# Kernel tuning notes

Measured on AMD Instinct MI355X. Metric: run time of the kernel, lower is better.

The kernel has to match this reference:

```python
import jax, jax.numpy as jnp
import numpy as np

SEQ, D_IN, D_OUT = 8192, 1024, 1024


def setup_inputs() -> dict:
    key = jax.random.key(0)
    kx, kq, kk, kv = jax.random.split(key, 4)
    # torch nn.Linear weights have shape (out_features, in_features)
    s = 1.0 / np.sqrt(D_IN)
    return {
        "x": jax.random.normal(kx, (SEQ, D_IN), dtype=jnp.float32),
        "Wq": jax.random.uniform(kq, (D_OUT, D_IN), dtype=jnp.float32, minval=-s, maxval=s),
        "Wk": jax.random.uniform(kk, (D_OUT, D_IN), dtype=jnp.float32, minval=-s, maxval=s),
        "Wv": jax.random.uniform(kv, (D_OUT, D_IN), dtype=jnp.float32, minval=-s, maxval=s),
    }


def reference(x, Wq, Wk, Wv):
    # Linear (no bias): y = x @ W.T
    q = x @ Wq.T          # [S, D_OUT]
    k = x @ Wk.T          # [S, D_OUT]
    v = x @ Wv.T          # [S, D_OUT]
    scale = 1.0 / jnp.sqrt(jnp.asarray(k.shape[-1], dtype=x.dtype))
    scores = (q @ k.T) * scale            # [S, S]
    weights = jax.nn.softmax(scores, axis=-1)
    return weights @ v                    # [S, D_OUT]
```

## Files before the change

### kernel.cpp

```cpp
#include <hip/hip_runtime.h>
#include <hip/hip_bf16.h>
#include <stdint.h>


#define SEQ 8192
#define DMODEL 1024
#define LOG2E 1.44269504088896340736f
#define GROUP_M 8

typedef __bf16 bf16_t;
typedef __bf16 bf16x8 __attribute__((ext_vector_type(8)));
typedef float f32x4 __attribute__((ext_vector_type(4)));

__global__ __launch_bounds__(256)
void convert_f32_bf16(const float* __restrict__ in, bf16_t* __restrict__ out, long n) {
    long i = ((long)blockIdx.x * 256 + threadIdx.x) * 4;
    if (i + 3 < n) {
        const float4 v = *(const float4*)(in + i);
        union { ushort4 u; bf16_t b[4]; } p;
        p.b[0] = (bf16_t)v.x; p.b[1] = (bf16_t)v.y;
        p.b[2] = (bf16_t)v.z; p.b[3] = (bf16_t)v.w;
        *(ushort4*)(out + i) = p.u;
    }
}

__global__ __launch_bounds__(256)
void add_f32(float* __restrict__ out, const float* __restrict__ part, long n) {
    long i = ((long)blockIdx.x * 256 + threadIdx.x) * 4;
    if (i + 3 < n) {
        float4 a = *(const float4*)(out + i);
        const float4 b = *(const float4*)(part + i);
        a.x += b.x; a.y += b.y; a.z += b.z; a.w += b.w;
        *(float4*)(out + i) = a;
    }
}

template <typename OutT>
__global__ __launch_bounds__(256, 3)
void gemm_nt(const bf16_t* __restrict__ A, const bf16_t* __restrict__ B,
             OutT* __restrict__ C0, OutT* __restrict__ C1,
             int M, int N, int Kps, int lda, int ldb, int ldc, float alpha)
{
    __shared__ bf16_t As[128 * 32];
    __shared__ bf16_t Bs[128 * 32];

    const int tid  = threadIdx.x;
    const int wave = tid >> 6;
    const int lane = tid & 63;

    const int nbm = M >> 7, nbn = N >> 7;
    const int tiles = nbm * nbn;
    int bid = blockIdx.x;
    const int sid = bid / tiles;
    bid -= sid * tiles;
    const long kbase = (long)sid * Kps;
    OutT* __restrict__ C = sid ? C1 : C0;

    const int per_group = GROUP_M * nbn;
    const int gid   = bid / per_group;
    const int rem   = bid - gid * per_group;
    const int first = gid * GROUP_M;
    const int gsz   = min(nbm - first, GROUP_M);
    const int bm    = first + rem % gsz;
    const int bn    = rem / gsz;
    const long row0 = (long)bm * 128;
    const long col0 = (long)bn * 128;

    const int wm = (wave >> 1) * 64;
    const int wn = (wave & 1) * 64;
    const int lr = lane & 15;
    const int lq = lane >> 4;

    f32x4 acc[4][4] = {};

    for (int k0 = 0; k0 < Kps; k0 += 32) {
        #pragma unroll
        for (int i = 0; i < 2; ++i) {
            const int cbase = i * 256 + wave * 64;
            const int c = cbase + lane;
            const int r = c >> 2, cc = c & 3;
            const bf16_t* ga = A + (row0 + r) * (long)lda + kbase + k0 + cc * 8;
            const bf16_t* gb = B + (col0 + r) * (long)ldb + kbase + k0 + cc * 8;
            __builtin_amdgcn_global_load_lds(
                (const __attribute__((address_space(1))) uint32_t*)ga,
                (__attribute__((address_space(3))) uint32_t*)(As + (long)cbase * 8),
                16, 0, 0);
            __builtin_amdgcn_global_load_lds(
                (const __attribute__((address_space(1))) uint32_t*)gb,
                (__attribute__((address_space(3))) uint32_t*)(Bs + (long)cbase * 8),
                16, 0, 0);
        }
        __syncthreads();

        bf16x8 af[4], bfr[4];
        #pragma unroll
        for (int mi = 0; mi < 4; ++mi)
            af[mi] = *(const bf16x8*)(As + (wm + mi * 16 + lr) * 32 + lq * 8);
        #pragma unroll
        for (int ni = 0; ni < 4; ++ni)
            bfr[ni] = *(const bf16x8*)(Bs + (wn + ni * 16 + lr) * 32 + lq * 8);

        #pragma unroll
        for (int mi = 0; mi < 4; ++mi)
            #pragma unroll
            for (int ni = 0; ni < 4; ++ni)
                acc[mi][ni] = __builtin_amdgcn_mfma_f32_16x16x32_bf16(
                    af[mi], bfr[ni], acc[mi][ni], 0, 0, 0);
        __syncthreads();
    }

    #pragma unroll
    for (int mi = 0; mi < 4; ++mi)
        #pragma unroll
        for (int ni = 0; ni < 4; ++ni)
            #pragma unroll
            for (int rg = 0; rg < 4; ++rg) {
                const long r = row0 + wm + mi * 16 + lq * 4 + rg;
                const long c = col0 + wn + ni * 16 + lr;
                C[r * (long)ldc + c] = (OutT)(alpha * acc[mi][ni][rg]);
            }
}

__global__ __launch_bounds__(256)
void transpose_bf16(const bf16_t* __restrict__ in, bf16_t* __restrict__ out,
                    int R, int ldin, int ldout)
{
    __shared__ bf16_t tile[32][33];
    const int tx = threadIdx.x & 31;
    const int ty = threadIdx.x >> 5;
    const int c0 = blockIdx.x * 32;
    const int r0 = blockIdx.y * 32;
    #pragma unroll
    for (int j = 0; j < 32; j += 8)
        tile[ty + j][tx] = in[(long)(r0 + ty + j) * ldin + c0 + tx];
    __syncthreads();
    #pragma unroll
    for (int j = 0; j < 32; j += 8)
        out[(long)(c0 + ty + j) * ldout + r0 + tx] = tile[tx][ty + j];
}

__global__ __launch_bounds__(256)
void softmax_rows(bf16_t* __restrict__ S, int n)
{
    const long row = blockIdx.x;
    bf16_t* p = S + row * (long)n;
    const int tid = threadIdx.x;
    const int wave = tid >> 6, lane = tid & 63;
    __shared__ float red[4];

    float v[32];
    #pragma unroll
    for (int j = 0; j < 4; ++j) {
        bf16x8 x = *(const bf16x8*)(p + ((long)(j * 256 + tid)) * 8);
        #pragma unroll
        for (int e = 0; e < 8; ++e) v[j * 8 + e] = (float)x[e];
    }
    float m = -3.4e38f;
    #pragma unroll
    for (int i = 0; i < 32; ++i) m = fmaxf(m, v[i]);
    #pragma unroll
    for (int off = 32; off > 0; off >>= 1) m = fmaxf(m, __shfl_xor(m, off));
    if (lane == 0) red[wave] = m;
    __syncthreads();
    m = fmaxf(fmaxf(red[0], red[1]), fmaxf(red[2], red[3]));
    __syncthreads();

    float s = 0.f;
    #pragma unroll
    for (int i = 0; i < 32; ++i) { v[i] = exp2f((v[i] - m) * LOG2E); s += v[i]; }
    #pragma unroll
    for (int off = 32; off > 0; off >>= 1) s += __shfl_xor(s, off);
    if (lane == 0) red[wave] = s;
    __syncthreads();
    s = red[0] + red[1] + red[2] + red[3];
    const float inv = 1.f / s;

    #pragma unroll
    for (int j = 0; j < 4; ++j) {
        bf16x8 x;
        #pragma unroll
        for (int e = 0; e < 8; ++e) x[e] = (bf16_t)(v[j * 8 + e] * inv);
        *(bf16x8*)(p + ((long)(j * 256 + tid)) * 8) = x;
    }
}

extern "C" void kernel_launch(void* const* d_in, const int* in_sizes, int n_in,
                              void* d_out, int out_size, void* d_ws, size_t ws_size,
                              hipStream_t stream)
{
    const float* x  = (const float*)d_in[0];
    const float* Wq = (const float*)d_in[1];
    const float* Wk = (const float*)d_in[2];
    const float* Wv = (const float*)d_in[3];
    float* out = (float*)d_out;

    char* ws = (char*)d_ws;
    const long XN = (long)SEQ * DMODEL;
    const long WN = (long)DMODEL * DMODEL;
    const long SN = (long)SEQ * SEQ;

    bf16_t* xb   = (bf16_t*)ws;
    bf16_t* wcat = (bf16_t*)(ws + XN * 2);
    bf16_t* qkv  = (bf16_t*)(ws + XN * 2 + WN * 6);
    bf16_t* Sb   = (bf16_t*)(ws + XN * 2 + WN * 6 + XN * 6);
    float*  pvp  = (float*)(ws + XN * 2 + WN * 6 + XN * 6 + SN * 2);
    bf16_t* vtb  = xb;

    const size_t need_split = (size_t)(XN * 2 + WN * 6 + XN * 6 + SN * 2) + XN * 4;
    const bool use_split = ws_size >= need_split;

    convert_f32_bf16<<<(int)(XN / 4 / 256), 256, 0, stream>>>(x,  xb, XN);
    convert_f32_bf16<<<(int)(WN / 4 / 256), 256, 0, stream>>>(Wq, wcat,          WN);
    convert_f32_bf16<<<(int)(WN / 4 / 256), 256, 0, stream>>>(Wk, wcat + WN,     WN);
    convert_f32_bf16<<<(int)(WN / 4 / 256), 256, 0, stream>>>(Wv, wcat + 2 * WN, WN);

    dim3 blk(256);
    gemm_nt<bf16_t><<<(SEQ / 128) * (3 * DMODEL / 128), blk, 0, stream>>>(
        xb, wcat, qkv, qkv, SEQ, 3 * DMODEL, DMODEL,
        DMODEL, DMODEL, 3 * DMODEL, 1.0f);

    bf16_t* qb = qkv;
    bf16_t* kb = qkv + DMODEL;
    bf16_t* vb = qkv + 2 * DMODEL;

    transpose_bf16<<<dim3(DMODEL / 32, SEQ / 32), blk, 0, stream>>>(
        vb, vtb, SEQ, 3 * DMODEL, SEQ);

    gemm_nt<bf16_t><<<(SEQ / 128) * (SEQ / 128), blk, 0, stream>>>(
        qb, kb, Sb, Sb, SEQ, SEQ, DMODEL,
        3 * DMODEL, 3 * DMODEL, SEQ, 0.03125f);

    softmax_rows<<<SEQ, blk, 0, stream>>>(Sb, SEQ);

    if (use_split) {
        gemm_nt<float><<<2 * (SEQ / 128) * (DMODEL / 128), blk, 0, stream>>>(
            Sb, vtb, out, pvp, SEQ, DMODEL, SEQ / 2,
            SEQ, SEQ, DMODEL, 1.0f);
        add_f32<<<(int)(XN / 4 / 256), 256, 0, stream>>>(out, pvp, XN);
    } else {
        gemm_nt<float><<<(SEQ / 128) * (DMODEL / 128), blk, 0, stream>>>(
            Sb, vtb, out, out, SEQ, DMODEL, SEQ,
            SEQ, SEQ, DMODEL, 1.0f);
    }
}
```

Baseline: 564.6 us.

## Compute QK^T scores with FP8 MFMA using e4m3 Q/K from fused QKV epilogue

The QKV projection kernel now writes Q and K as FP8 e4m3 and V as bf16 into separate planes. A new FP8 GEMM then computes the 8192x8192 score matrix using the fp8 16x16x32 MFMA with 64-wide K tiles. The aim is to double the math throughput and halve the operand bandwidth of the largest GEMM. In exchange, FP8 precision for Q and K reduces score accuracy, and there is no per-tensor scaling.

```diff
diff --git a/kernel.cpp b/kernel.cpp
--- a/kernel.cpp
+++ b/kernel.cpp
@@ -11,6 +11,11 @@
 typedef __bf16 bf16_t;
 typedef __bf16 bf16x8 __attribute__((ext_vector_type(8)));
 typedef float f32x4 __attribute__((ext_vector_type(4)));
+
+__device__ __forceinline__ uint8_t f32_to_e4m3(float v) {
+    int p = __builtin_amdgcn_cvt_pk_fp8_f32(v, 0.0f, 0, false);
+    return (uint8_t)(p & 0xff);
+}
 
 __global__ __launch_bounds__(256)
 void convert_f32_bf16(const float* __restrict__ in, bf16_t* __restrict__ out, long n) {
@@ -35,6 +40,172 @@
     }
 }
 
+__global__ __launch_bounds__(256, 3)
+void gemm_qkv(const bf16_t* __restrict__ A, const bf16_t* __restrict__ B,
+              uint8_t* __restrict__ qf8, uint8_t* __restrict__ kf8,
+              bf16_t* __restrict__ vb)
+{
+    __shared__ bf16_t As[128 * 32];
+    __shared__ bf16_t Bs[128 * 32];
+
+    const int tid  = threadIdx.x;
+    const int wave = tid >> 6;
+    const int lane = tid & 63;
+
+    const int nbm = SEQ >> 7, nbn = (3 * DMODEL) >> 7;
+    const int per_group = GROUP_M * nbn;
+    const int gid   = blockIdx.x / per_group;
+    const int rem   = blockIdx.x - gid * per_group;
+    const int first = gid * GROUP_M;
+    const int gsz   = min(nbm - first, GROUP_M);
+    const int bm    = first + rem % gsz;
+    const int bn    = rem / gsz;
+    const long row0 = (long)bm * 128;
+    const long col0 = (long)bn * 128;
+
+    const int wm = (wave >> 1) * 64;
+    const int wn = (wave & 1) * 64;
+    const int lr = lane & 15;
+    const int lq = lane >> 4;
+
+    f32x4 acc[4][4] = {};
+
+    for (int k0 = 0; k0 < DMODEL; k0 += 32) {
+        #pragma unroll
+        for (int i = 0; i < 2; ++i) {
+            const int cbase = i * 256 + wave * 64;
+            const int c = cbase + lane;
+            const int r = c >> 2, cc = c & 3;
+            const bf16_t* ga = A + (row0 + r) * (long)DMODEL + k0 + cc * 8;
+            const bf16_t* gb = B + (col0 + r) * (long)DMODEL + k0 + cc * 8;
+            __builtin_amdgcn_global_load_lds(
+                (const __attribute__((address_space(1))) uint32_t*)ga,
+                (__attribute__((address_space(3))) uint32_t*)(As + (long)cbase * 8),
+                16, 0, 0);
+            __builtin_amdgcn_global_load_lds(
+                (const __attribute__((address_space(1))) uint32_t*)gb,
+                (__attribute__((address_space(3))) uint32_t*)(Bs + (long)cbase * 8),
+                16, 0, 0);
+        }
+        __syncthreads();
+
+        bf16x8 af[4], bfr[4];
+        #pragma unroll
+        for (int mi = 0; mi < 4; ++mi)
+            af[mi] = *(const bf16x8*)(As + (wm + mi * 16 + lr) * 32 + lq * 8);
+        #pragma unroll
+        for (int ni = 0; ni < 4; ++ni)
+            bfr[ni] = *(const bf16x8*)(Bs + (wn + ni * 16 + lr) * 32 + lq * 8);
+
+        #pragma unroll
+        for (int mi = 0; mi < 4; ++mi)
+            #pragma unroll
+            for (int ni = 0; ni < 4; ++ni)
+                acc[mi][ni] = __builtin_amdgcn_mfma_f32_16x16x32_bf16(
+                    af[mi], bfr[ni], acc[mi][ni], 0, 0, 0);
+        __syncthreads();
+    }
+
+    const int plane = (int)(col0 >> 10);
+    const int cb    = (int)(col0 & 1023);
+    #pragma unroll
+    for (int mi = 0; mi < 4; ++mi)
+        #pragma unroll
+        for (int ni = 0; ni < 4; ++ni)
+            #pragma unroll
+            for (int rg = 0; rg < 4; ++rg) {
+                const long r = row0 + wm + mi * 16 + lq * 4 + rg;
+                const int  c = cb + wn + ni * 16 + lr;
+                const float val = acc[mi][ni][rg];
+                if (plane == 2)
+                    vb[r * (long)DMODEL + c] = (bf16_t)val;
+                else if (plane == 1)
+                    kf8[r * (long)DMODEL + c] = f32_to_e4m3(val);
+                else
+                    qf8[r * (long)DMODEL + c] = f32_to_e4m3(val);
+            }
+}
+
+__global__ __launch_bounds__(256, 3)
+void gemm_s_fp8(const uint8_t* __restrict__ A, const uint8_t* __restrict__ B,
+                bf16_t* __restrict__ C, float alpha)
+{
+    __shared__ uint8_t As[128 * 64];
+    __shared__ uint8_t Bs[128 * 64];
+
+    const int tid  = threadIdx.x;
+    const int wave = tid >> 6;
+    const int lane = tid & 63;
+
+    const int nbm = SEQ >> 7, nbn = SEQ >> 7;
+    const int per_group = GROUP_M * nbn;
+    const int gid   = blockIdx.x / per_group;
+    const int rem   = blockIdx.x - gid * per_group;
+    const int first = gid * GROUP_M;
+    const int gsz   = min(nbm - first, GROUP_M);
+    const int bm    = first + rem % gsz;
+    const int bn    = rem / gsz;
+    const long row0 = (long)bm * 128;
+    const long col0 = (long)bn * 128;
+
+    const int wm = (wave >> 1) * 64;
+    const int wn = (wave & 1) * 64;
+    const int lr = lane & 15;
+    const int lq = lane >> 4;
+
+    f32x4 acc[4][4] = {};
+
+    for (int k0 = 0; k0 < DMODEL; k0 += 64) {
+        #pragma unroll
+        for (int i = 0; i < 2; ++i) {
+            const int cbase = i * 256 + wave * 64;
+            const int c = cbase + lane;
+            const int r = c >> 2, cc = c & 3;
+            const uint8_t* ga = A + (row0 + r) * (long)DMODEL + k0 + cc * 16;
+            const uint8_t* gb = B + (col0 + r) * (long)DMODEL + k0 + cc * 16;
+            __builtin_amdgcn_global_load_lds(
+                (const __attribute__((address_space(1))) uint32_t*)ga,
+                (__attribute__((address_space(3))) uint32_t*)(As + (long)cbase * 16),
+                16, 0, 0);
+            __builtin_amdgcn_global_load_lds(
+                (const __attribute__((address_space(1))) uint32_t*)gb,
+                (__attribute__((address_space(3))) uint32_t*)(Bs + (long)cbase * 16),
+                16, 0, 0);
+        }
+        __syncthreads();
+
+        #pragma unroll
+        for (int t = 0; t < 2; ++t) {
+            long af[4], bfr[4];
+            #pragma unroll
+            for (int mi = 0; mi < 4; ++mi)
+                af[mi] = *(const long*)(As + (wm + mi * 16 + lr) * 64 + t * 32 + lq * 8);
+            #pragma unroll
+            for (int ni = 0; ni < 4; ++ni)
+                bfr[ni] = *(const long*)(Bs + (wn + ni * 16 + lr) * 64 + t * 32 + lq * 8);
+
+            #pragma unroll
+            for (int mi = 0; mi < 4; ++mi)
+                #pragma unroll
+                for (int ni = 0; ni < 4; ++ni)
+                    acc[mi][ni] = __builtin_amdgcn_mfma_f32_16x16x32_fp8_fp8(
+                        af[mi], bfr[ni], acc[mi][ni], 0, 0, 0);
+        }
+        __syncthreads();
+    }
+
+    #pragma unroll
+    for (int mi = 0; mi < 4; ++mi)
+        #pragma unroll
+        for (int ni = 0; ni < 4; ++ni)
+            #pragma unroll
+            for (int rg = 0; rg < 4; ++rg) {
+                const long r = row0 + wm + mi * 16 + lq * 4 + rg;
+                const long c = col0 + wn + ni * 16 + lr;
+                C[r * (long)SEQ + c] = (bf16_t)(alpha * acc[mi][ni][rg]);
+            }
+}
+
 template <typename OutT>
 __global__ __launch_bounds__(256, 3)
 void gemm_nt(const bf16_t* __restrict__ A, const bf16_t* __restrict__ B,
@@ -201,12 +372,14 @@
 
     bf16_t* xb   = (bf16_t*)ws;
     bf16_t* wcat = (bf16_t*)(ws + XN * 2);
-    bf16_t* qkv  = (bf16_t*)(ws + XN * 2 + WN * 6);
-    bf16_t* Sb   = (bf16_t*)(ws + XN * 2 + WN * 6 + XN * 6);
-    float*  pvp  = (float*)(ws + XN * 2 + WN * 6 + XN * 6 + SN * 2);
+    uint8_t* qf8 = (uint8_t*)(ws + XN * 2 + WN * 6);
+    uint8_t* kf8 = qf8 + XN;
+    bf16_t* vb   = (bf16_t*)(ws + XN * 2 + WN * 6 + XN * 2);
+    bf16_t* Sb   = (bf16_t*)(ws + XN * 2 + WN * 6 + XN * 4);
+    float*  pvp  = (float*)(ws + XN * 2 + WN * 6 + XN * 4 + SN * 2);
     bf16_t* vtb  = xb;
 
-    const size_t need_split = (size_t)(XN * 2 + WN * 6 + XN * 6 + SN * 2) + XN * 4;
+    const size_t need_split = (size_t)(XN * 2 + WN * 6 + XN * 4 + SN * 2) + XN * 4;
     const bool use_split = ws_size >= need_split;
 
     convert_f32_bf16<<<(int)(XN / 4 / 256), 256, 0, stream>>>(x,  xb, XN);
@@ -215,20 +388,14 @@
     convert_f32_bf16<<<(int)(WN / 4 / 256), 256, 0, stream>>>(Wv, wcat + 2 * WN, WN);
 
     dim3 blk(256);
-    gemm_nt<bf16_t><<<(SEQ / 128) * (3 * DMODEL / 128), blk, 0, stream>>>(
-        xb, wcat, qkv, qkv, SEQ, 3 * DMODEL, DMODEL,
-        DMODEL, DMODEL, 3 * DMODEL, 1.0f);
-
-    bf16_t* qb = qkv;
-    bf16_t* kb = qkv + DMODEL;
-    bf16_t* vb = qkv + 2 * DMODEL;
+    gemm_qkv<<<(SEQ / 128) * (3 * DMODEL / 128), blk, 0, stream>>>(
+        xb, wcat, qf8, kf8, vb);
 
     transpose_bf16<<<dim3(DMODEL / 32, SEQ / 32), blk, 0, stream>>>(
-        vb, vtb, SEQ, 3 * DMODEL, SEQ);
-
-    gemm_nt<bf16_t><<<(SEQ / 128) * (SEQ / 128), blk, 0, stream>>>(
-        qb, kb, Sb, Sb, SEQ, SEQ, DMODEL,
-        3 * DMODEL, 3 * DMODEL, SEQ, 0.03125f);
+        vb, vtb, SEQ, DMODEL, SEQ);
+
+    gemm_s_fp8<<<(SEQ / 128) * (SEQ / 128), blk, 0, stream>>>(
+        qf8, kf8, Sb, 0.03125f);
 
     softmax_rows<<<SEQ, blk, 0, stream>>>(Sb, SEQ);
 
```

Measured after the change: 605.2 us. 7.2% more time.
